# Optimization experiments

Measured on AMD Instinct MI355X. Metric: run time of the kernel, lower is better.

The kernel has to match this reference:

```python
import jax, jax.numpy as jnp
import numpy as np

# Static problem constants (must match setup_inputs)
NUM_GRAPHS = 64      # batch_size = int(batch[-1]) + 1
PTS_PER_GRAPH = 512
RATIO = 16           # centroids per graph
HEADS = 4
IN_CH = 64           # = out_channels per head (concat=False -> mean over heads)
NEG_SLOPE = 0.2


def setup_inputs() -> dict:
    key = jax.random.key(0)
    ks = jax.random.split(key, 8)
    N = NUM_GRAPHS * PTS_PER_GRAPH
    x = jax.random.normal(ks[0], (N, IN_CH), dtype=jnp.float32)
    edge_index = jnp.zeros((2, 2), dtype=jnp.int64)  # unused by forward
    batch = (jnp.arange(N) // PTS_PER_GRAPH).astype(jnp.int64)
    xcent_base = jax.random.normal(ks[1], (RATIO, IN_CH), dtype=jnp.float32)
    W_l = jax.random.normal(ks[2], (IN_CH, HEADS * IN_CH), dtype=jnp.float32) / np.sqrt(IN_CH)
    b_l = jax.random.normal(ks[3], (HEADS * IN_CH,), dtype=jnp.float32) * 0.01
    W_r = jax.random.normal(ks[4], (IN_CH, HEADS * IN_CH), dtype=jnp.float32) / np.sqrt(IN_CH)
    b_r = jax.random.normal(ks[5], (HEADS * IN_CH,), dtype=jnp.float32) * 0.01
    att = jax.random.normal(ks[6], (HEADS, IN_CH), dtype=jnp.float32) / np.sqrt(IN_CH)
    bias = jax.random.normal(ks[7], (IN_CH,), dtype=jnp.float32) * 0.01
    return {"x": x, "edge_index": edge_index, "batch": batch,
            "xcent_base": xcent_base, "W_l": W_l, "b_l": b_l,
            "W_r": W_r, "b_r": b_r, "att": att, "bias": bias}


def _bipart_pool(x, batch, xcent_base, W_l, b_l, W_r, b_r, att, bias):
    N = x.shape[0]
    B = NUM_GRAPHS
    Nc = B * RATIO  # number of centroid (target) nodes

    # Dense bipartite edges: each source node -> all RATIO centroids of its graph.
    src = jnp.repeat(jnp.arange(N, dtype=jnp.int32), RATIO)                     # [E]
    dst = jnp.tile(jnp.arange(RATIO, dtype=jnp.int32), N) \
        + jnp.repeat(batch.astype(jnp.int32), RATIO) * RATIO                    # [E]

    # PyG GATv2Conv(add_self_loops=True): remove src==dst edges, then add
    # self loops (i,i) for i < min(N_src, N_dst) = Nc. Keep static shapes by
    # masking the removed edges instead of deleting them.
    self_idx = jnp.arange(Nc, dtype=jnp.int32)
    src_f = jnp.concatenate([src, self_idx])
    dst_f = jnp.concatenate([dst, self_idx])
    drop = jnp.concatenate([src == dst, jnp.zeros((Nc,), dtype=bool)])          # [E+Nc]

    # Linear projections (source and target sides)
    x_l = (x @ W_l + b_l).reshape(N, HEADS, IN_CH)                              # [N,H,C]
    xcent = jnp.tile(xcent_base, (B, 1))                                        # [Nc,IN]
    x_r = (xcent @ W_r + b_r).reshape(Nc, HEADS, IN_CH)                         # [Nc,H,C]

    # GATv2 attention: leaky_relu(x_i + x_j) . att, softmax per target node
    xj = x_l[src_f]                                                             # [E',H,C]
    g = jax.nn.leaky_relu(xj + x_r[dst_f], NEG_SLOPE)
    alpha = jnp.einsum('ehc,hc->eh', g, att)                                    # [E',H]
    alpha = jnp.where(drop[:, None], jnp.float32(-1e30), alpha)
    amax = jax.ops.segment_max(alpha, dst_f, num_segments=Nc)                   # [Nc,H]
    e = jnp.exp(alpha - amax[dst_f])
    den = jax.ops.segment_sum(e, dst_f, num_segments=Nc)                        # [Nc,H]
    w = e / den[dst_f]                                                          # [E',H]

    out = jax.ops.segment_sum(w[..., None] * xj, dst_f, num_segments=Nc)        # [Nc,H,C]
    out = out.mean(axis=1) + bias                                               # concat=False -> mean heads
    return out.reshape(B, RATIO, IN_CH)


def reference(x, edge_index, batch, xcent_base, W_l, b_l, W_r, b_r, att, bias):
    xcent = _bipart_pool(x, batch, xcent_base, W_l, b_l, W_r, b_r, att, bias)
    batchcent = jnp.repeat(jnp.arange(NUM_GRAPHS, dtype=jnp.int64), RATIO)
    return xcent, batchcent
```

## Files before the change

### kernel.cpp

```cpp
#include <hip/hip_runtime.h>

#define PTS 512
#define CH  64

using s8v = __attribute__((ext_vector_type(8))) short;
using f4v = __attribute__((ext_vector_type(4))) float;

static __device__ __forceinline__ unsigned short f2b(float f) {
    unsigned u = __float_as_uint(f);
    return (unsigned short)((u + 0x7FFFu + ((u >> 16) & 1u)) >> 16);
}

__global__ __launch_bounds__(256) void k0(
    const float* __restrict__ xcb, const float* __restrict__ W_r,
    const float* __restrict__ b_r, const float* __restrict__ att,
    const float* __restrict__ bias,
    float* __restrict__ xr_ws, float* __restrict__ sxr_ws,
    float* __restrict__ out)
{
    __shared__ float s_row[256];
    const int blk = blockIdx.x, tid = threadIdx.x;
    if (blk < 16) {
        const int h = blk >> 2, rq = blk & 3;
        const int rl = tid >> 6, c = tid & 63;
        const int r = rq * 4 + rl;
        float acc = b_r[h * 64 + c];
        for (int k = 0; k < 64; ++k)
            acc = fmaf(xcb[r * 64 + k], W_r[k * 256 + h * 64 + c], acc);
        xr_ws[(h * 16 + r) * 64 + c] = acc;
        s_row[rl * 64 + c] = acc;
        __syncthreads();
        if (tid < 4) {
            float s = 0.f;
            for (int cc = 0; cc < 64; ++cc)
                s = fmaf(s_row[tid * 64 + cc], att[h * 64 + cc], s);
            sxr_ws[h * 16 + rq * 4 + tid] = s;
        }
    } else if (blk < 32) {
        const int base = (blk - 16) * 4096;
        float4 bv = *(const float4*)(bias + ((tid * 4) & 63));
#pragma unroll
        for (int j = 0; j < 4; ++j)
            *(float4*)(out + base + j * 1024 + tid * 4) = bv;
    } else {
        const int c = tid * 4;
        *(float4*)(out + 65536 + c) = make_float4(
            (float)(c >> 4), (float)((c + 1) >> 4),
            (float)((c + 2) >> 4), (float)((c + 3) >> 4));
    }
}

__global__ __launch_bounds__(512, 1) void kmain(
    const float* __restrict__ x, const float* __restrict__ W_l,
    const float* __restrict__ b_l, const float* __restrict__ att,
    const float* __restrict__ xr_ws, const float* __restrict__ sxr_ws,
    float* __restrict__ out)
{
    __shared__ __align__(16) float s_buf[16384];
    __shared__ __align__(16) float s_alpha[8192];
    __shared__ __align__(16) unsigned short s_wt[4096];
    __shared__ float s_W[4096];
    __shared__ float s_xls[1024];
    __shared__ float s_aself[16], s_m[16], s_inv[16], s_f[16];

    unsigned short* s_xl   = (unsigned short*)s_buf;
    float*          s_part = s_buf;
    float*          s_y    = s_buf + 8192;

    const int tid = threadIdx.x;
    const int h = blockIdx.x >> 6;
    const int b = blockIdx.x & 63;
    const int lane = tid & 63;
    const int w = __builtin_amdgcn_readfirstlane(tid >> 6);

    {
        const int c = tid >> 3, kk0 = (tid & 7) * 8;
        s8v wv;
#pragma unroll
        for (int j = 0; j < 8; ++j)
            wv[j] = (short)f2b(W_l[(kk0 + j) * 256 + h * 64 + c]);
        *(s8v*)&s_wt[c * 64 + (kk0 ^ ((c & 7) << 3))] = wv;

        for (int idx = tid; idx < 4096; idx += 512)
            s_W[idx] = W_l[(idx >> 6) * 256 + h * 64 + (idx & 63)];
    }
    __syncthreads();

    {
        const int r0 = w * 2;
        const float* xg0 = x + (size_t)(b * 16 + r0) * 64;
        const float* xg1 = xg0 + 64;
        float a0 = b_l[h * 64 + lane];
        float a1 = a0;
        for (int k = 0; k < 64; ++k) {
            const float wv = s_W[k * 64 + lane];
            a0 = fmaf(xg0[k], wv, a0);
            a1 = fmaf(xg1[k], wv, a1);
        }
        s_xls[r0 * 64 + lane] = a0;
        s_xls[(r0 + 1) * 64 + lane] = a1;

        const float at = att[h * 64 + lane];
        float sx0 = at * a0, ab0 = at * fabsf(a0 + xr_ws[(h * 16 + r0) * 64 + lane]);
        float sx1 = at * a1, ab1 = at * fabsf(a1 + xr_ws[(h * 16 + r0 + 1) * 64 + lane]);
#pragma unroll
        for (int off = 32; off >= 1; off >>= 1) {
            sx0 += __shfl_xor(sx0, off); ab0 += __shfl_xor(ab0, off);
            sx1 += __shfl_xor(sx1, off); ab1 += __shfl_xor(ab1, off);
        }
        if (lane == 0) {
            s_aself[r0]     = 0.6f * (sx0 + sxr_ws[h * 16 + r0])     + 0.4f * ab0;
            s_aself[r0 + 1] = 0.6f * (sx1 + sxr_ws[h * 16 + r0 + 1]) + 0.4f * ab1;
        }
    }

    {
        const int l15 = lane & 15, quad = lane >> 4;
        const size_t row0 = (size_t)b * PTS + w * 64;
        f4v acc[4][4];
        const f4v zf = {0.f, 0.f, 0.f, 0.f};
#pragma unroll
        for (int m = 0; m < 4; ++m)
#pragma unroll
            for (int n = 0; n < 4; ++n) acc[m][n] = zf;

#pragma unroll
        for (int ks = 0; ks < 2; ++ks) {
            s8v Af[4], Bf[4];
#pragma unroll
            for (int m = 0; m < 4; ++m) {
                const float* xp = x + (row0 + m * 16 + l15) * 64 + ks * 32 + quad * 8;
                float4 u0 = *(const float4*)xp;
                float4 u1 = *(const float4*)(xp + 4);
                s8v a;
                a[0] = (short)f2b(u0.x); a[1] = (short)f2b(u0.y);
                a[2] = (short)f2b(u0.z); a[3] = (short)f2b(u0.w);
                a[4] = (short)f2b(u1.x); a[5] = (short)f2b(u1.y);
                a[6] = (short)f2b(u1.z); a[7] = (short)f2b(u1.w);
                Af[m] = a;
            }
#pragma unroll
            for (int n = 0; n < 4; ++n) {
                const int cc = n * 16 + l15;
                Bf[n] = *(const s8v*)&s_wt[cc * 64 +
                        ((ks * 32 + quad * 8) ^ ((cc & 7) << 3))];
            }
#pragma unroll
            for (int m = 0; m < 4; ++m)
#pragma unroll
                for (int n = 0; n < 4; ++n)
                    acc[m][n] = __builtin_amdgcn_mfma_f32_16x16x32_bf16(
                        Af[m], Bf[n], acc[m][n], 0, 0, 0);
        }

        float blv[4];
#pragma unroll
        for (int n = 0; n < 4; ++n) blv[n] = b_l[h * 64 + n * 16 + l15];
#pragma unroll
        for (int m = 0; m < 4; ++m)
#pragma unroll
            for (int n = 0; n < 4; ++n) {
                const int cc = n * 16 + l15;
#pragma unroll
                for (int qq = 0; qq < 4; ++qq) {
                    const int row = w * 64 + m * 16 + quad * 4 + qq;
                    s_xl[row * 64 + (cc ^ ((row & 7) << 3))] =
                        f2b(acc[m][n][qq] + blv[n]);
                }
            }
    }
    __syncthreads();

    {
        const int i = tid, sw = i & 3, xsw = (i & 7) << 3;
        const float* attw = att + h * 64;
        const float* xrw  = xr_ws + h * 1024;
        float ac[16];
#pragma unroll
        for (int r = 0; r < 16; ++r) ac[r] = 0.f;
        float sxl = 0.f;

#pragma unroll
        for (int half = 0; half < 2; ++half) {
            const int cb = half * 32;
            float xlv[32], atv[32];
#pragma unroll
            for (int c8 = 0; c8 < 4; ++c8) {
                const int ch0 = cb + c8 * 8;
                uint4 raw = *(const uint4*)&s_xl[i * 64 + (ch0 ^ xsw)];
                unsigned uu[4] = {raw.x, raw.y, raw.z, raw.w};
#pragma unroll
                for (int p = 0; p < 4; ++p) {
                    xlv[c8 * 8 + 2 * p]     = __uint_as_float(uu[p] << 16);
                    xlv[c8 * 8 + 2 * p + 1] = __uint_as_float(uu[p] & 0xffff0000u);
                }
            }
#pragma unroll
            for (int cq = 0; cq < 8; ++cq) {
                float4 a4 = *(const float4*)(attw + cb + cq * 4);
                atv[cq * 4 + 0] = a4.x; atv[cq * 4 + 1] = a4.y;
                atv[cq * 4 + 2] = a4.z; atv[cq * 4 + 3] = a4.w;
            }
#pragma unroll
            for (int t = 0; t < 32; ++t) sxl = fmaf(atv[t], xlv[t], sxl);

#pragma unroll 2
            for (int r = 0; r < 16; ++r) {
                const float4* xrp = (const float4*)(xrw + r * 64 + cb);
                float a = 0.f;
#pragma unroll
                for (int cq = 0; cq < 8; ++cq) {
                    float4 x4 = xrp[cq];
                    a = fmaf(atv[cq * 4 + 0], fabsf(xlv[cq * 4 + 0] + x4.x), a);
                    a = fmaf(atv[cq * 4 + 1], fabsf(xlv[cq * 4 + 1] + x4.y), a);
                    a = fmaf(atv[cq * 4 + 2], fabsf(xlv[cq * 4 + 2] + x4.z), a);
                    a = fmaf(atv[cq * 4 + 3], fabsf(xlv[cq * 4 + 3] + x4.w), a);
                }
                ac[r] += a;
            }
        }
        float av[16];
#pragma unroll
        for (int r = 0; r < 16; ++r)
            av[r] = 0.6f * (sxl + sxr_ws[h * 16 + r]) + 0.4f * ac[r];
        float4* sa4 = (float4*)s_alpha;
#pragma unroll
        for (int q = 0; q < 4; ++q) {
            float4 v = make_float4(av[q * 4 + 0], av[q * 4 + 1],
                                   av[q * 4 + 2], av[q * 4 + 3]);
            sa4[i * 4 + (q ^ sw)] = v;
        }
    }
    __syncthreads();

    {
        const int r = tid >> 5, lg = tid & 31;
        const float a_self = s_aself[r];
        float m = a_self;
        for (int j = 0; j < 16; ++j) {
            const int i = lg + j * 32;
            float a = s_alpha[(i << 4) + (r ^ ((i & 3) << 2))];
            if (b == 0 && i == r) a = -1e30f;
            m = fmaxf(m, a);
        }
#pragma unroll
        for (int off = 16; off >= 1; off >>= 1) m = fmaxf(m, __shfl_xor(m, off));
        float d = 0.f;
        for (int j = 0; j < 16; ++j) {
            const int i = lg + j * 32;
            float a = s_alpha[(i << 4) + (r ^ ((i & 3) << 2))];
            d += (b == 0 && i == r) ? 0.f : __expf(a - m);
        }
#pragma unroll
        for (int off = 16; off >= 1; off >>= 1) d += __shfl_xor(d, off);
        if (lg == 0) {
            const float es = __expf(a_self - m);
            const float inv = 1.f / (d + es);
            s_m[r] = m; s_inv[r] = inv; s_f[r] = es * inv;
        }
    }
    __syncthreads();

    {
        const int i = tid, sw = i & 3;
        float4* sa4 = (float4*)s_alpha;
#pragma unroll
        for (int p = 0; p < 4; ++p) {
            float4 v = sa4[i * 4 + p];
            const int r0 = (p ^ sw) * 4;
            v.x = (b == 0 && i == r0 + 0) ? 0.f : __expf(v.x - s_m[r0 + 0]) * s_inv[r0 + 0];
            v.y = (b == 0 && i == r0 + 1) ? 0.f : __expf(v.y - s_m[r0 + 1]) * s_inv[r0 + 1];
            v.z = (b == 0 && i == r0 + 2) ? 0.f : __expf(v.z - s_m[r0 + 2]) * s_inv[r0 + 2];
            v.w = (b == 0 && i == r0 + 3) ? 0.f : __expf(v.w - s_m[r0 + 3]) * s_inv[r0 + 3];
            sa4[i * 4 + p] = v;
        }
    }
    __syncthreads();

    {
        const int kt = tid & 15, rt = (tid >> 4) & 3, is = tid >> 6;
        float y4[4][4];
#pragma unroll
        for (int i = 0; i < 4; ++i)
#pragma unroll
            for (int j = 0; j < 4; ++j) y4[i][j] = 0.f;

        const float* xb = x + ((size_t)b * PTS + is * 64) * 64;
        const float4* sa4 = (const float4*)s_alpha;
#pragma unroll 4
        for (int ii = 0; ii < 64; ++ii) {
            float4 xv = *(const float4*)(xb + ii * 64 + kt * 4);
            const int i = is * 64 + ii;
            float4 ev = sa4[i * 4 + (rt ^ (i & 3))];
            y4[0][0] = fmaf(ev.x, xv.x, y4[0][0]); y4[0][1] = fmaf(ev.x, xv.y, y4[0][1]);
            y4[0][2] = fmaf(ev.x, xv.z, y4[0][2]); y4[0][3] = fmaf(ev.x, xv.w, y4[0][3]);
            y4[1][0] = fmaf(ev.y, xv.x, y4[1][0]); y4[1][1] = fmaf(ev.y, xv.y, y4[1][1]);
            y4[1][2] = fmaf(ev.y, xv.z, y4[1][2]); y4[1][3] = fmaf(ev.y, xv.w, y4[1][3]);
            y4[2][0] = fmaf(ev.z, xv.x, y4[2][0]); y4[2][1] = fmaf(ev.z, xv.y, y4[2][1]);
            y4[2][2] = fmaf(ev.z, xv.z, y4[2][2]); y4[2][3] = fmaf(ev.z, xv.w, y4[2][3]);
            y4[3][0] = fmaf(ev.w, xv.x, y4[3][0]); y4[3][1] = fmaf(ev.w, xv.y, y4[3][1]);
            y4[3][2] = fmaf(ev.w, xv.z, y4[3][2]); y4[3][3] = fmaf(ev.w, xv.w, y4[3][3]);
        }
#pragma unroll
        for (int rr = 0; rr < 4; ++rr)
            *(float4*)&s_part[is * 1024 + (rt * 4 + rr) * 64 + kt * 4] =
                make_float4(y4[rr][0], y4[rr][1], y4[rr][2], y4[rr][3]);
    }
    __syncthreads();

    for (int o = tid; o < 1024; o += 512) {
        float s = 0.f;
#pragma unroll
        for (int sl = 0; sl < 8; ++sl) s += s_part[sl * 1024 + o];
        s_y[o] = s;
    }
    __syncthreads();

    for (int o = tid; o < 1024; o += 512) {
        const int r = o >> 6, ch = o & 63;
        float a = 0.f;
        const float* yr = s_y + r * 64;
#pragma unroll
        for (int k = 0; k < 64; ++k)
            a = fmaf(yr[k], s_W[k * 64 + ch], a);
        const float f = s_f[r];
        float val = a + (1.f - f) * b_l[h * 64 + ch] + f * s_xls[r * 64 + ch];
        atomicAdd(&out[(b * 16 + r) * 64 + ch], 0.25f * val);
    }
}

extern "C" void kernel_launch(void* const* d_in, const int* in_sizes, int n_in,
                              void* d_out, int out_size, void* d_ws, size_t ws_size,
                              hipStream_t stream) {
    (void)in_sizes; (void)n_in; (void)out_size; (void)ws_size;
    const float* x    = (const float*)d_in[0];
    const float* xcb  = (const float*)d_in[3];
    const float* W_l  = (const float*)d_in[4];
    const float* b_l  = (const float*)d_in[5];
    const float* W_r  = (const float*)d_in[6];
    const float* b_r  = (const float*)d_in[7];
    const float* att  = (const float*)d_in[8];
    const float* bias = (const float*)d_in[9];
    float* out = (float*)d_out;

    float* wsf = (float*)d_ws;
    float* xr_ws  = wsf;
    float* sxr_ws = wsf + 4096;

    hipLaunchKernelGGL(k0, dim3(33), dim3(256), 0, stream,
                       xcb, W_r, b_r, att, bias, xr_ws, sxr_ws, out);
    hipLaunchKernelGGL(kmain, dim3(256), dim3(512), 0, stream,
                       x, W_l, b_l, att, xr_ws, sxr_ws, out);
}
```

Before: 113.1 us.

## Drop softmax max pass, defer normalization, and reuse bf16 weights for self rows

Computes exp of the attention logits directly, without subtracting the per-target max. The unnormalized exponentials are stored while denominators are reduced with wave shuffles, and the division is applied once at the final output. This removes two barrier-separated passes over the alpha buffer and the fp32 copy of W_l in LDS. The self-row projection now reads the bf16 transposed weights, and the final projection reads W_l from global memory. The risks are overflow in exp without max subtraction, lower precision in the self-row projection, and slower global reads for the final weight access.

```diff
diff --git a/kernel.cpp b/kernel.cpp
--- a/kernel.cpp
+++ b/kernel.cpp
@@ -9,6 +9,9 @@
 static __device__ __forceinline__ unsigned short f2b(float f) {
     unsigned u = __float_as_uint(f);
     return (unsigned short)((u + 0x7FFFu + ((u >> 16) & 1u)) >> 16);
+}
+static __device__ __forceinline__ float b2f(unsigned short s) {
+    return __uint_as_float((unsigned)s << 16);
 }
 
 __global__ __launch_bounds__(256) void k0(
@@ -57,15 +60,15 @@
     float* __restrict__ out)
 {
     __shared__ __align__(16) float s_buf[16384];
-    __shared__ __align__(16) float s_alpha[8192];
+    __shared__ __align__(16) float s_e[8192];
     __shared__ __align__(16) unsigned short s_wt[4096];
-    __shared__ float s_W[4096];
-    __shared__ float s_xls[1024];
-    __shared__ float s_aself[16], s_m[16], s_inv[16], s_f[16];
+    __shared__ __align__(16) float s_xls[1024];
+    __shared__ __align__(16) float s_y[1024];
+    __shared__ float s_dpart[128];
+    __shared__ float s_es[16], s_dns[16], s_inv[16];
 
     unsigned short* s_xl   = (unsigned short*)s_buf;
     float*          s_part = s_buf;
-    float*          s_y    = s_buf + 8192;
 
     const int tid = threadIdx.x;
     const int h = blockIdx.x >> 6;
@@ -80,9 +83,6 @@
         for (int j = 0; j < 8; ++j)
             wv[j] = (short)f2b(W_l[(kk0 + j) * 256 + h * 64 + c]);
         *(s8v*)&s_wt[c * 64 + (kk0 ^ ((c & 7) << 3))] = wv;
-
-        for (int idx = tid; idx < 4096; idx += 512)
-            s_W[idx] = W_l[(idx >> 6) * 256 + h * 64 + (idx & 63)];
     }
     __syncthreads();
 
@@ -90,12 +90,16 @@
         const int r0 = w * 2;
         const float* xg0 = x + (size_t)(b * 16 + r0) * 64;
         const float* xg1 = xg0 + 64;
-        float a0 = b_l[h * 64 + lane];
-        float a1 = a0;
-        for (int k = 0; k < 64; ++k) {
-            const float wv = s_W[k * 64 + lane];
-            a0 = fmaf(xg0[k], wv, a0);
-            a1 = fmaf(xg1[k], wv, a1);
+        float a0 = b_l[h * 64 + lane], a1 = a0;
+#pragma unroll
+        for (int j8 = 0; j8 < 8; ++j8) {
+            s8v wraw = *(const s8v*)&s_wt[lane * 64 + ((j8 * 8) ^ ((lane & 7) << 3))];
+#pragma unroll
+            for (int j = 0; j < 8; ++j) {
+                const float wvf = b2f((unsigned short)wraw[j]);
+                a0 = fmaf(xg0[j8 * 8 + j], wvf, a0);
+                a1 = fmaf(xg1[j8 * 8 + j], wvf, a1);
+            }
         }
         s_xls[r0 * 64 + lane] = a0;
         s_xls[(r0 + 1) * 64 + lane] = a1;
@@ -109,8 +113,8 @@
             sx1 += __shfl_xor(sx1, off); ab1 += __shfl_xor(ab1, off);
         }
         if (lane == 0) {
-            s_aself[r0]     = 0.6f * (sx0 + sxr_ws[h * 16 + r0])     + 0.4f * ab0;
-            s_aself[r0 + 1] = 0.6f * (sx1 + sxr_ws[h * 16 + r0 + 1]) + 0.4f * ab1;
+            s_es[r0]     = __expf(0.6f * (sx0 + sxr_ws[h * 16 + r0])     + 0.4f * ab0);
+            s_es[r0 + 1] = __expf(0.6f * (sx1 + sxr_ws[h * 16 + r0 + 1]) + 0.4f * ab1);
         }
     }
 
@@ -219,63 +223,37 @@
                 ac[r] += a;
             }
         }
-        float av[16];
-#pragma unroll
-        for (int r = 0; r < 16; ++r)
-            av[r] = 0.6f * (sxl + sxr_ws[h * 16 + r]) + 0.4f * ac[r];
-        float4* sa4 = (float4*)s_alpha;
-#pragma unroll
-        for (int q = 0; q < 4; ++q) {
-            float4 v = make_float4(av[q * 4 + 0], av[q * 4 + 1],
-                                   av[q * 4 + 2], av[q * 4 + 3]);
-            sa4[i * 4 + (q ^ sw)] = v;
-        }
-    }
-    __syncthreads();
-
-    {
-        const int r = tid >> 5, lg = tid & 31;
-        const float a_self = s_aself[r];
-        float m = a_self;
-        for (int j = 0; j < 16; ++j) {
-            const int i = lg + j * 32;
-            float a = s_alpha[(i << 4) + (r ^ ((i & 3) << 2))];
-            if (b == 0 && i == r) a = -1e30f;
-            m = fmaxf(m, a);
-        }
-#pragma unroll
-        for (int off = 16; off >= 1; off >>= 1) m = fmaxf(m, __shfl_xor(m, off));
-        float d = 0.f;
-        for (int j = 0; j < 16; ++j) {
-            const int i = lg + j * 32;
-            float a = s_alpha[(i << 4) + (r ^ ((i & 3) << 2))];
-            d += (b == 0 && i == r) ? 0.f : __expf(a - m);
-        }
-#pragma unroll
-        for (int off = 16; off >= 1; off >>= 1) d += __shfl_xor(d, off);
-        if (lg == 0) {
-            const float es = __expf(a_self - m);
-            const float inv = 1.f / (d + es);
-            s_m[r] = m; s_inv[r] = inv; s_f[r] = es * inv;
-        }
-    }
-    __syncthreads();
-
-    {
-        const int i = tid, sw = i & 3;
-        float4* sa4 = (float4*)s_alpha;
-#pragma unroll
-        for (int p = 0; p < 4; ++p) {
-            float4 v = sa4[i * 4 + p];
-            const int r0 = (p ^ sw) * 4;
-            v.x = (b == 0 && i == r0 + 0) ? 0.f : __expf(v.x - s_m[r0 + 0]) * s_inv[r0 + 0];
-            v.y = (b == 0 && i == r0 + 1) ? 0.f : __expf(v.y - s_m[r0 + 1]) * s_inv[r0 + 1];
-            v.z = (b == 0 && i == r0 + 2) ? 0.f : __expf(v.z - s_m[r0 + 2]) * s_inv[r0 + 2];
-            v.w = (b == 0 && i == r0 + 3) ? 0.f : __expf(v.w - s_m[r0 + 3]) * s_inv[r0 + 3];
-            sa4[i * 4 + p] = v;
-        }
-    }
-    __syncthreads();
+        float ev[16];
+#pragma unroll
+        for (int r = 0; r < 16; ++r) {
+            float a = 0.6f * (sxl + sxr_ws[h * 16 + r]) + 0.4f * ac[r];
+            float e = __expf(a);
+            if (b == 0 && i == r) e = 0.f;
+            ev[r] = e;
+        }
+        float4* se4 = (float4*)s_e;
+#pragma unroll
+        for (int q = 0; q < 4; ++q)
+            se4[i * 4 + (q ^ sw)] = make_float4(ev[q * 4 + 0], ev[q * 4 + 1],
+                                                ev[q * 4 + 2], ev[q * 4 + 3]);
+#pragma unroll
+        for (int r = 0; r < 16; ++r) {
+            float s = ev[r];
+#pragma unroll
+            for (int off = 32; off >= 1; off >>= 1) s += __shfl_xor(s, off);
+            if (lane == 0) s_dpart[w * 16 + r] = s;
+        }
+    }
+    __syncthreads();
+
+    if (tid < 16) {
+        float dns = 0.f;
+#pragma unroll
+        for (int ww = 0; ww < 8; ++ww) dns += s_dpart[ww * 16 + tid];
+        const float es = s_es[tid];
+        s_dns[tid] = dns;
+        s_inv[tid] = 1.f / (dns + es);
+    }
 
     {
         const int kt = tid & 15, rt = (tid >> 4) & 3, is = tid >> 6;
@@ -286,20 +264,29 @@
             for (int j = 0; j < 4; ++j) y4[i][j] = 0.f;
 
         const float* xb = x + ((size_t)b * PTS + is * 64) * 64;
-        const float4* sa4 = (const float4*)s_alpha;
-#pragma unroll 4
-        for (int ii = 0; ii < 64; ++ii) {
-            float4 xv = *(const float4*)(xb + ii * 64 + kt * 4);
-            const int i = is * 64 + ii;
-            float4 ev = sa4[i * 4 + (rt ^ (i & 3))];
-            y4[0][0] = fmaf(ev.x, xv.x, y4[0][0]); y4[0][1] = fmaf(ev.x, xv.y, y4[0][1]);
-            y4[0][2] = fmaf(ev.x, xv.z, y4[0][2]); y4[0][3] = fmaf(ev.x, xv.w, y4[0][3]);
-            y4[1][0] = fmaf(ev.y, xv.x, y4[1][0]); y4[1][1] = fmaf(ev.y, xv.y, y4[1][1]);
-            y4[1][2] = fmaf(ev.y, xv.z, y4[1][2]); y4[1][3] = fmaf(ev.y, xv.w, y4[1][3]);
-            y4[2][0] = fmaf(ev.z, xv.x, y4[2][0]); y4[2][1] = fmaf(ev.z, xv.y, y4[2][1]);
-            y4[2][2] = fmaf(ev.z, xv.z, y4[2][2]); y4[2][3] = fmaf(ev.z, xv.w, y4[2][3]);
-            y4[3][0] = fmaf(ev.w, xv.x, y4[3][0]); y4[3][1] = fmaf(ev.w, xv.y, y4[3][1]);
-            y4[3][2] = fmaf(ev.w, xv.z, y4[3][2]); y4[3][3] = fmaf(ev.w, xv.w, y4[3][3]);
+        const float4* se4 = (const float4*)s_e;
+        for (int ii0 = 0; ii0 < 64; ii0 += 8) {
+            float4 xv[8], evv[8];
+#pragma unroll
+            for (int u = 0; u < 8; ++u)
+                xv[u] = *(const float4*)(xb + (ii0 + u) * 64 + kt * 4);
+#pragma unroll
+            for (int u = 0; u < 8; ++u) {
+                const int i = is * 64 + ii0 + u;
+                evv[u] = se4[i * 4 + (rt ^ (i & 3))];
+            }
+#pragma unroll
+            for (int u = 0; u < 8; ++u) {
+                const float4 xvu = xv[u], ev = evv[u];
+                y4[0][0] = fmaf(ev.x, xvu.x, y4[0][0]); y4[0][1] = fmaf(ev.x, xvu.y, y4[0][1]);
+                y4[0][2] = fmaf(ev.x, xvu.z, y4[0][2]); y4[0][3] = fmaf(ev.x, xvu.w, y4[0][3]);
+                y4[1][0] = fmaf(ev.y, xvu.x, y4[1][0]); y4[1][1] = fmaf(ev.y, xvu.y, y4[1][1]);
+                y4[1][2] = fmaf(ev.y, xvu.z, y4[1][2]); y4[1][3] = fmaf(ev.y, xvu.w, y4[1][3]);
+                y4[2][0] = fmaf(ev.z, xvu.x, y4[2][0]); y4[2][1] = fmaf(ev.z, xvu.y, y4[2][1]);
+                y4[2][2] = fmaf(ev.z, xvu.z, y4[2][2]); y4[2][3] = fmaf(ev.z, xvu.w, y4[2][3]);
+                y4[3][0] = fmaf(ev.w, xvu.x, y4[3][0]); y4[3][1] = fmaf(ev.w, xvu.y, y4[3][1]);
+                y4[3][2] = fmaf(ev.w, xvu.z, y4[3][2]); y4[3][3] = fmaf(ev.w, xvu.w, y4[3][3]);
+            }
         }
 #pragma unroll
         for (int rr = 0; rr < 4; ++rr)
@@ -322,9 +309,9 @@
         const float* yr = s_y + r * 64;
 #pragma unroll
         for (int k = 0; k < 64; ++k)
-            a = fmaf(yr[k], s_W[k * 64 + ch], a);
-        const float f = s_f[r];
-        float val = a + (1.f - f) * b_l[h * 64 + ch] + f * s_xls[r * 64 + ch];
+            a = fmaf(yr[k], W_l[k * 256 + h * 64 + ch], a);
+        float val = (a + s_dns[r] * b_l[h * 64 + ch]
+                     + s_es[r] * s_xls[r * 64 + ch]) * s_inv[r];
         atomicAdd(&out[(b * 16 + r) * 64 + ch], 0.25f * val);
     }
 }
```

Result: no change. 111.5 us (median of 2 runs) (-1.4%).
